# Optimization experiments

Hardware: AMD Instinct MI355X
Metric: run time of the kernel (lower is better)

## Reference

```python
import jax, jax.numpy as jnp
import numpy as np

H = 64  # hidden size


def _gru_cell(x, h, Wih, Whh, bih, bhh):
    """PyTorch-convention GRU cell. x:[B,in], h:[B,H]. Gate order: r, z, n."""
    gi = x @ Wih.T + bih              # [B, 3H]
    gh = h @ Whh.T + bhh              # [B, 3H]
    ir, iz, in_ = jnp.split(gi, 3, axis=-1)
    hr, hz, hn = jnp.split(gh, 3, axis=-1)
    r = jax.nn.sigmoid(ir + hr)
    z = jax.nn.sigmoid(iz + hz)
    n = jnp.tanh(in_ + r * hn)
    return (1.0 - z) * n + z * h


def setup_inputs() -> dict:
    key = jax.random.key(0)
    B, T, NIN = 4096, 256, 6
    ks = jax.random.split(key, 24)

    def w(k, shape, fan):
        return (jax.random.normal(k, shape, jnp.float32) / np.sqrt(fan).astype(np.float32))

    inp = {"x": jax.random.normal(ks[0], (B, T, NIN), jnp.float32)}
    # encoder layer 0 (input 6) and layer 1 (input 64)
    inp["enc_Wih0"] = w(ks[1], (3 * H, NIN), H)
    inp["enc_Whh0"] = w(ks[2], (3 * H, H), H)
    inp["enc_bih0"] = w(ks[3], (3 * H,), H)
    inp["enc_bhh0"] = w(ks[4], (3 * H,), H)
    inp["enc_Wih1"] = w(ks[5], (3 * H, H), H)
    inp["enc_Whh1"] = w(ks[6], (3 * H, H), H)
    inp["enc_bih1"] = w(ks[7], (3 * H,), H)
    inp["enc_bhh1"] = w(ks[8], (3 * H,), H)
    # decoder layer 0 (input 1) and layer 1 (input 64)
    inp["dec_Wih0"] = w(ks[9], (3 * H, 1), H)
    inp["dec_Whh0"] = w(ks[10], (3 * H, H), H)
    inp["dec_bih0"] = w(ks[11], (3 * H,), H)
    inp["dec_bhh0"] = w(ks[12], (3 * H,), H)
    inp["dec_Wih1"] = w(ks[13], (3 * H, H), H)
    inp["dec_Whh1"] = w(ks[14], (3 * H, H), H)
    inp["dec_bih1"] = w(ks[15], (3 * H,), H)
    inp["dec_bhh1"] = w(ks[16], (3 * H,), H)
    # output head
    inp["out_W"] = w(ks[17], (1, H), H)
    inp["out_b"] = w(ks[18], (1,), H)
    inp["target_len"] = 180
    return inp


def reference(x, enc_Wih0, enc_Whh0, enc_bih0, enc_bhh0,
              enc_Wih1, enc_Whh1, enc_bih1, enc_bhh1,
              dec_Wih0, dec_Whh0, dec_bih0, dec_bhh0,
              dec_Wih1, dec_Whh1, dec_bih1, dec_bhh1,
              out_W, out_b, target_len):
    B = x.shape[0]
    dtype = x.dtype

    # ---- encoder: 2-layer GRU over x, return final hidden per layer ----
    seq = jnp.swapaxes(x, 0, 1)  # [T, B, 6] time-major
    enc_layers = [(enc_Wih0, enc_Whh0, enc_bih0, enc_bhh0),
                  (enc_Wih1, enc_Whh1, enc_bih1, enc_bhh1)]
    h_finals = []
    for (Wih, Whh, bih, bhh) in enc_layers:
        def step(h, xt, Wih=Wih, Whh=Whh, bih=bih, bhh=bhh):
            hn = _gru_cell(xt, h, Wih, Whh, bih, bhh)
            return hn, hn
        h_last, seq = jax.lax.scan(step, jnp.zeros((B, H), dtype), seq)
        h_finals.append(h_last)

    def dec_step(carry, _):
        h0, h1, prev = carry
        h0 = _gru_cell(prev, h0, dec_Wih0, dec_Whh0, dec_bih0, dec_bhh0)
        h1 = _gru_cell(h0, h1, dec_Wih1, dec_Whh1, dec_bih1, dec_bhh1)
        cv = h1 @ out_W.T + out_b  # [B, 1]
        return (h0, h1, cv), cv

    prev0 = jnp.zeros((B, 1), dtype)
    _, outs = jax.lax.scan(dec_step, (h_finals[0], h_finals[1], prev0),
                           None, length=target_len)
    return jnp.swapaxes(outs, 0, 1)  # [B, target_len, 1]
```

## Files before the change

### kernel.cpp

```cpp
#include <hip/hip_runtime.h>
#include <cstdint>

typedef _Float16 half8 __attribute__((ext_vector_type(8)));
typedef __attribute__((ext_vector_type(4))) float floatx4;
typedef unsigned int uint;

#define TSEQ 256
#define TDEC 180
#define NIN  6
#define GROWS 16
#define NBLK (4096 / GROWS)
#define NSL 4
#define RS0 104
#define RS1 72
#define L2E 1.4426950408889634f

__device__ __forceinline__ floatx4 mfma16(half8 a, half8 b, floatx4 c) {
  return __builtin_amdgcn_mfma_f32_16x16x32_f16(a, b, c, 0, 0, 0);
}

__device__ __forceinline__ float sigm2(float v) {
  return __builtin_amdgcn_rcpf(1.0f + __builtin_amdgcn_exp2f(-v));
}
__device__ __forceinline__ float tanh2(float v) {
  return fmaf(2.0f, __builtin_amdgcn_rcpf(1.0f + __builtin_amdgcn_exp2f(-v)), -1.0f);
}

__device__ __forceinline__ half8 ldh8(const _Float16* p) { return *(const half8*)p; }

#define PASS2_I3(F0, F1, r, z, g, W, QR, QZ, QG) do {                   \
  r = mfma16(F0, W[0][0], QR); z = mfma16(F0, W[1][0], QZ); g = mfma16(F0, W[2][0], QG); \
  r = mfma16(F1, W[0][1], r);  z = mfma16(F1, W[1][1], z);  g = mfma16(F1, W[2][1], g);  \
} while (0)

#define PASS2_A2I1(F0, F1, r, z, g, W, QG) do {                         \
  r = mfma16(F0, W[0][0], r); z = mfma16(F0, W[1][0], z); g = mfma16(F0, W[2][0], QG); \
  r = mfma16(F1, W[0][1], r); z = mfma16(F1, W[1][1], z); g = mfma16(F1, W[2][1], g);  \
} while (0)

#define PASS1_A2I1(F0, r, z, g, W, QG) do {                             \
  r = mfma16(F0, W[0][0], r); z = mfma16(F0, W[1][0], z); g = mfma16(F0, W[2][0], QG); \
} while (0)

__device__ __forceinline__ void pollge1(const volatile uint* p, uint need4) {
  for (;;) {
    if (*p >= need4) break;
    __builtin_amdgcn_s_sleep(1);
  }
  asm volatile("" ::: "memory");
}

#define PUBLISH() do { asm volatile("" ::: "memory"); if (lane == 0) atomicAdd(mysum, 1u); } while (0)

__global__ void __launch_bounds__(512, 2)
gru_persist(const float* __restrict__ x,
            const float* __restrict__ eWih0, const float* __restrict__ eWhh0,
            const float* __restrict__ ebih0, const float* __restrict__ ebhh0,
            const float* __restrict__ eWih1, const float* __restrict__ eWhh1,
            const float* __restrict__ ebih1, const float* __restrict__ ebhh1,
            const float* __restrict__ dWih0, const float* __restrict__ dWhh0,
            const float* __restrict__ dbih0, const float* __restrict__ dbhh0,
            const float* __restrict__ dWih1, const float* __restrict__ dWhh1,
            const float* __restrict__ dbih1, const float* __restrict__ dbhh1,
            const float* __restrict__ outW, const float* __restrict__ outB,
            float* __restrict__ out)
{
  __shared__ __align__(16) _Float16 s0[NSL][16][RS0];
  __shared__ __align__(16) _Float16 s1[NSL][16][RS1];
  __shared__ __align__(16) uint prog[16];

  const int tid  = threadIdx.x;
  const bool isA = tid < 256;
  const int wvL  = (tid >> 6) & 3;
  const int lane = tid & 63;
  const int c    = lane & 15;
  const int q    = lane >> 4;
  const int u    = wvL * 16 + c;
  const long base = (long)blockIdx.x * GROWS;

  const volatile uint* asum = (const volatile uint*)&prog[0];
  const volatile uint* bsum = (const volatile uint*)&prog[8];
  uint* mysum = (uint*)&prog[isA ? 0 : 8];

  for (int i = tid; i < NSL * 16 * RS0; i += 512) ((uint16_t*)s0)[i] = 0;
  for (int i = tid; i < NSL * 16 * RS1; i += 512) ((uint16_t*)s1)[i] = 0;
  if (tid < 16) prog[tid] = 0;
  if (tid < GROWS * NIN) {
    int m = tid / 6, i2 = tid - m * 6;
    s0[0][m][64 + i2] = (_Float16)x[(base + m) * (TSEQ * NIN) + i2];
  }

  half8 W1[3][2], W2[3][2];
  half8 W1d[3][2], W2d[3][2];
  float hr[4] = {0, 0, 0, 0};
  const float SC[3] = {L2E, L2E, 2.0f * L2E};

  auto loadW64 = [&](const float* W, half8 (&D)[3][2]) {
    #pragma unroll
    for (int s = 0; s < 3; s++) {
      const int n = (s * 4 + wvL) * 16 + c;
      #pragma unroll
      for (int kt = 0; kt < 2; kt++) {
        const int k0 = kt * 32 + q * 8;
        #pragma unroll
        for (int j = 0; j < 8; j++) D[s][kt][j] = (_Float16)(SC[s] * W[n * 64 + k0 + j]);
      }
    }
  };

  const float ob = outB[0];
  float cR, cZ, c3, c4;
  float dR, dZ, d3, d4;
  float bR0 = 0, bZ0 = 0, b30 = 0, b40 = 0;
  float wk[2][8];
  if (isA) {
    loadW64(eWhh0, W1);
    #pragma unroll
    for (int s = 0; s < 3; s++) {
      const int n = (s * 4 + wvL) * 16 + c;
      #pragma unroll
      for (int kt = 0; kt < 2; kt++)
        #pragma unroll
        for (int j = 0; j < 8; j++) {
          float v = (kt == 0 && q == 0 && j < NIN) ? SC[s] * eWih0[n * NIN + j] : 0.0f;
          W2[s][kt][j] = (_Float16)v;
        }
    }
    loadW64(dWhh0, W1d);
    #pragma unroll
    for (int s = 0; s < 3; s++) {
      const int n = (s * 4 + wvL) * 16 + c;
      const float wd = SC[s] * dWih0[n];
      #pragma unroll
      for (int kt = 0; kt < 2; kt++) {
        const int k0 = kt * 32 + q * 8;
        #pragma unroll
        for (int j = 0; j < 8; j++) W2d[s][kt][j] = (_Float16)(wd * outW[k0 + j]);
      }
    }
    cR = L2E * (ebih0[u] + ebhh0[u]);
    cZ = L2E * (ebih0[64 + u] + ebhh0[64 + u]);
    c3 = 2.0f * L2E * ebhh0[128 + u];
    c4 = 2.0f * L2E * ebih0[128 + u];
    bR0 = L2E * (dbih0[u] + dbhh0[u]);
    bZ0 = L2E * (dbih0[64 + u] + dbhh0[64 + u]);
    b30 = 2.0f * L2E * dbhh0[128 + u];
    b40 = 2.0f * L2E * dbih0[128 + u];
    dR = bR0 + L2E * (dWih0[u] * ob);
    dZ = bZ0 + L2E * (dWih0[64 + u] * ob);
    d3 = b30;
    d4 = b40 + 2.0f * L2E * (dWih0[128 + u] * ob);
  } else {
    loadW64(eWih1, W1); loadW64(eWhh1, W2);
    loadW64(dWih1, W1d); loadW64(dWhh1, W2d);
    cR = L2E * (ebih1[u] + ebhh1[u]);
    cZ = L2E * (ebih1[64 + u] + ebhh1[64 + u]);
    c3 = 2.0f * L2E * ebih1[128 + u];
    c4 = 2.0f * L2E * ebhh1[128 + u];
    dR = L2E * (dbih1[u] + dbhh1[u]);
    dZ = L2E * (dbih1[64 + u] + dbhh1[64 + u]);
    d3 = 2.0f * L2E * dbih1[128 + u];
    d4 = 2.0f * L2E * dbhh1[128 + u];
    #pragma unroll
    for (int kt = 0; kt < 2; kt++)
      #pragma unroll
      for (int j = 0; j < 8; j++) wk[kt][j] = outW[kt * 32 + q * 8 + j];
  }
  __syncthreads();

  if (isA) {
    floatx4 QR = {cR, cR, cR, cR}, QZ = {cZ, cZ, cZ, cZ};
    floatx4 Q3 = {c3, c3, c3, c3}, Q4 = {c4, c4, c4, c4};
    const bool doX = (wvL == 0) && (lane < 48);
    const float *px0 = nullptr, *px1 = nullptr;
    int xo0 = 0, xo1 = 0;
    float xa0 = 0.f, xa1 = 0.f, xb0 = 0.f, xb1 = 0.f;
    if (doX) {
      int s0_ = lane, s1_ = lane + 48;
      int m0 = s0_ / 6, i0 = s0_ - m0 * 6, m1 = s1_ / 6, i1 = s1_ - m1 * 6;
      px0 = x + (base + m0) * (TSEQ * NIN) + i0;
      px1 = x + (base + m1) * (TSEQ * NIN) + i1;
      xo0 = m0 * RS0 + 64 + i0; xo1 = m1 * RS0 + 64 + i1;
      xa0 = px0[NIN];     xa1 = px1[NIN];
      xb0 = px0[2 * NIN]; xb1 = px1[2 * NIN];
    }
    for (int i = 0; i < TSEQ; i += 4) {
      #pragma unroll
      for (int h4 = 0; h4 < 4; h4++) {
        const int i_ = i + h4, p = h4, pn = (h4 + 1) & 3;
        pollge1(asum, 4u * (uint)i_);
        const half8 a0 = ldh8(&s0[p][c][q * 8]);
        const half8 a1 = ldh8(&s0[p][c][32 + q * 8]);
        const half8 xf = ldh8(&s0[p][c][64 + q * 8]);
        floatx4 aR, aZ, a3, a4;
        PASS2_I3(a0, a1, aR, aZ, a3, W1, QR, QZ, Q3);
        PASS1_A2I1(xf, aR, aZ, a4, W2, Q4);
        pollge1(bsum, 4u * (uint)(i_ > 3 ? i_ - 3 : 0));
        if (doX && i_ + 1 < TSEQ) {
          ((_Float16*)s0[pn])[xo0] = (_Float16)xa0;
          ((_Float16*)s0[pn])[xo1] = (_Float16)xa1;
          xa0 = xb0; xa1 = xb1;
          if (i_ + 3 < TSEQ) { xb0 = px0[(i_ + 3) * NIN]; xb1 = px1[(i_ + 3) * NIN]; }
        }
        #pragma unroll
        for (int r4 = 0; r4 < 4; r4++) {
          const float gr = sigm2(aR[r4]);
          const float gz = sigm2(aZ[r4]);
          const float nn = tanh2(a4[r4] + gr * a3[r4]);
          const float hn = nn + gz * (hr[r4] - nn);
          hr[r4] = hn;
          s0[pn][q * 4 + r4][u] = (_Float16)hn;
        }
        PUBLISH();
      }
    }
    QR = (floatx4){dR, dR, dR, dR}; QZ = (floatx4){dZ, dZ, dZ, dZ};
    Q3 = (floatx4){d3, d3, d3, d3}; Q4 = (floatx4){d4, d4, d4, d4};
    {
      pollge1(asum, 4u * (uint)TSEQ);
      const half8 a0 = ldh8(&s0[0][c][q * 8]);
      const half8 a1 = ldh8(&s0[0][c][32 + q * 8]);
      const floatx4 TR = {bR0, bR0, bR0, bR0}, TZ = {bZ0, bZ0, bZ0, bZ0};
      const floatx4 T3 = {b30, b30, b30, b30};
      floatx4 aR, aZ, a3;
      floatx4 a4 = {b40, b40, b40, b40};
      PASS2_I3(a0, a1, aR, aZ, a3, W1d, TR, TZ, T3);
      pollge1(bsum, 4u * (uint)(TSEQ - 1));
      #pragma unroll
      for (int r4 = 0; r4 < 4; r4++) {
        const float gr = sigm2(aR[r4]);
        const float gz = sigm2(aZ[r4]);
        const float nn = tanh2(a4[r4] + gr * a3[r4]);
        const float hn = nn + gz * (hr[r4] - nn);
        hr[r4] = hn;
        s0[1][q * 4 + r4][u] = (_Float16)hn;
      }
      PUBLISH();
    }
    for (int i_ = TSEQ + 1; i_ < TSEQ + TDEC; i_++) {
      const int p = i_ & 3, pn = (i_ + 1) & 3;
      pollge1(asum, 4u * (uint)i_);
      const half8 a0 = ldh8(&s0[p][c][q * 8]);
      const half8 a1 = ldh8(&s0[p][c][32 + q * 8]);
      floatx4 aR, aZ, a3, a4;
      PASS2_I3(a0, a1, aR, aZ, a3, W1d, QR, QZ, Q3);
      pollge1(bsum, 4u * (uint)i_);
      const half8 b0 = ldh8(&s1[p][c][q * 8]);
      const half8 b1 = ldh8(&s1[p][c][32 + q * 8]);
      PASS2_A2I1(b0, b1, aR, aZ, a4, W2d, Q4);
      #pragma unroll
      for (int r4 = 0; r4 < 4; r4++) {
        const float gr = sigm2(aR[r4]);
        const float gz = sigm2(aZ[r4]);
        const float nn = tanh2(a4[r4] + gr * a3[r4]);
        const float hn = nn + gz * (hr[r4] - nn);
        hr[r4] = hn;
        s0[pn][q * 4 + r4][u] = (_Float16)hn;
      }
      PUBLISH();
    }
  } else {
    floatx4 QR = {cR, cR, cR, cR}, QZ = {cZ, cZ, cZ, cZ};
    floatx4 Q3 = {c3, c3, c3, c3}, Q4 = {c4, c4, c4, c4};
    for (int i = 0; i < TSEQ; i += 4) {
      #pragma unroll
      for (int h4 = 0; h4 < 4; h4++) {
        const int i_ = i + h4, p = h4, pn = (h4 + 1) & 3;
        pollge1(bsum, 4u * (uint)i_);
        const half8 f0 = ldh8(&s1[p][c][q * 8]);
        const half8 f1 = ldh8(&s1[p][c][32 + q * 8]);
        floatx4 aR, aZ, a3, a4;
        PASS2_I3(f0, f1, aR, aZ, a4, W2, QR, QZ, Q4);
        pollge1(asum, 4u * (uint)(i_ + 1));
        const half8 g0 = ldh8(&s0[pn][c][q * 8]);
        const half8 g1 = ldh8(&s0[pn][c][32 + q * 8]);
        PASS2_A2I1(g0, g1, aR, aZ, a3, W1, Q3);
        #pragma unroll
        for (int r4 = 0; r4 < 4; r4++) {
          const float gr = sigm2(aR[r4]);
          const float gz = sigm2(aZ[r4]);
          const float nn = tanh2(a3[r4] + gr * a4[r4]);
          const float hn = nn + gz * (hr[r4] - nn);
          hr[r4] = hn;
          s1[pn][q * 4 + r4][u] = (_Float16)hn;
        }
        PUBLISH();
      }
    }
    QR = (floatx4){dR, dR, dR, dR}; QZ = (floatx4){dZ, dZ, dZ, dZ};
    Q3 = (floatx4){d3, d3, d3, d3}; Q4 = (floatx4){d4, d4, d4, d4};
    for (int i_ = TSEQ; i_ < TSEQ + TDEC; i_++) {
      const int p = i_ & 3, pn = (i_ + 1) & 3;
      pollge1(bsum, 4u * (uint)i_);
      const half8 f0 = ldh8(&s1[p][c][q * 8]);
      const half8 f1 = ldh8(&s1[p][c][32 + q * 8]);
      floatx4 aR, aZ, a3, a4;
      PASS2_I3(f0, f1, aR, aZ, a4, W2d, QR, QZ, Q4);
      if (wvL == 0 && i_ > TSEQ) {
        float cv = 0.0f;
        #pragma unroll
        for (int j = 0; j < 8; j++) {
          cv = fmaf((float)f0[j], wk[0][j], cv);
          cv = fmaf((float)f1[j], wk[1][j], cv);
        }
        cv += __shfl_xor(cv, 16);
        cv += __shfl_xor(cv, 32);
        if (lane < 16) out[(base + lane) * TDEC + (i_ - TSEQ - 1)] = cv + ob;
      }
      pollge1(asum, 4u * (uint)(i_ + 1));
      const half8 g0 = ldh8(&s0[pn][c][q * 8]);
      const half8 g1 = ldh8(&s0[pn][c][32 + q * 8]);
      PASS2_A2I1(g0, g1, aR, aZ, a3, W1d, Q3);
      #pragma unroll
      for (int r4 = 0; r4 < 4; r4++) {
        const float gr = sigm2(aR[r4]);
        const float gz = sigm2(aZ[r4]);
        const float nn = tanh2(a3[r4] + gr * a4[r4]);
        const float hn = nn + gz * (hr[r4] - nn);
        hr[r4] = hn;
        s1[pn][q * 4 + r4][u] = (_Float16)hn;
      }
      PUBLISH();
    }
    if (wvL == 0) {
      pollge1(bsum, 4u * (uint)(TSEQ + TDEC));
      const half8 f0 = ldh8(&s1[0][c][q * 8]);
      const half8 f1 = ldh8(&s1[0][c][32 + q * 8]);
      float cv = 0.0f;
      #pragma unroll
      for (int j = 0; j < 8; j++) {
        cv = fmaf((float)f0[j], wk[0][j], cv);
        cv = fmaf((float)f1[j], wk[1][j], cv);
      }
      cv += __shfl_xor(cv, 16);
      cv += __shfl_xor(cv, 32);
      if (lane < 16) out[(base + lane) * TDEC + (TDEC - 1)] = cv + ob;
    }
  }
}

extern "C" void kernel_launch(void* const* d_in, const int* in_sizes, int n_in,
                              void* d_out, int out_size, void* d_ws, size_t ws_size,
                              hipStream_t stream) {
  (void)in_sizes; (void)n_in; (void)d_ws; (void)ws_size; (void)out_size;
  const float* x     = (const float*)d_in[0];
  const float* eWih0 = (const float*)d_in[1];
  const float* eWhh0 = (const float*)d_in[2];
  const float* ebih0 = (const float*)d_in[3];
  const float* ebhh0 = (const float*)d_in[4];
  const float* eWih1 = (const float*)d_in[5];
  const float* eWhh1 = (const float*)d_in[6];
  const float* ebih1 = (const float*)d_in[7];
  const float* ebhh1 = (const float*)d_in[8];
  const float* dWih0 = (const float*)d_in[9];
  const float* dWhh0 = (const float*)d_in[10];
  const float* dbih0 = (const float*)d_in[11];
  const float* dbhh0 = (const float*)d_in[12];
  const float* dWih1 = (const float*)d_in[13];
  const float* dWhh1 = (const float*)d_in[14];
  const float* dbih1 = (const float*)d_in[15];
  const float* dbhh1 = (const float*)d_in[16];
  const float* outW  = (const float*)d_in[17];
  const float* outB  = (const float*)d_in[18];
  hipLaunchKernelGGL(gru_persist, dim3(NBLK), dim3(512), 0, stream,
                     x, eWih0, eWhh0, ebih0, ebhh0, eWih1, eWhh1, ebih1, ebhh1,
                     dWih0, dWhh0, dbih0, dbhh0, dWih1, dWhh1, dbih1, dbhh1,
                     outW, outB, (float*)d_out);
}
```

Measured before the change: 387.2 us.

## Replace LDS counter polling with workgroup barriers in a lockstep wavefront schedule

Drops the shared-memory progress counters, the sleep-polling loops and the atomic publishes between the layer-0 and layer-1 wave groups. All 8 waves now advance in lockstep with s_barrier, and the layer-1 schedule is skewed by one step through peeled prologue and epilogue iterations, so that matching barrier counts line up between the two groups. This removes atomic and polling latency, but loses the slack that let layer 0 run up to several steps ahead of layer 1. Mismatched barrier counts between the two branches would deadlock or race.

```diff
diff --git a/kernel.cpp b/kernel.cpp
--- a/kernel.cpp
+++ b/kernel.cpp
@@ -3,7 +3,6 @@
 
 typedef _Float16 half8 __attribute__((ext_vector_type(8)));
 typedef __attribute__((ext_vector_type(4))) float floatx4;
-typedef unsigned int uint;
 
 #define TSEQ 256
 #define TDEC 180
@@ -42,15 +41,11 @@
   r = mfma16(F0, W[0][0], r); z = mfma16(F0, W[1][0], z); g = mfma16(F0, W[2][0], QG); \
 } while (0)
 
-__device__ __forceinline__ void pollge1(const volatile uint* p, uint need4) {
-  for (;;) {
-    if (*p >= need4) break;
-    __builtin_amdgcn_s_sleep(1);
-  }
-  asm volatile("" ::: "memory");
-}
-
-#define PUBLISH() do { asm volatile("" ::: "memory"); if (lane == 0) atomicAdd(mysum, 1u); } while (0)
+#define SYNC() do {                                         \
+  asm volatile("s_waitcnt lgkmcnt(0)" ::: "memory");        \
+  __builtin_amdgcn_s_barrier();                             \
+  asm volatile("" ::: "memory");                            \
+} while (0)
 
 __global__ void __launch_bounds__(512, 2)
 gru_persist(const float* __restrict__ x,
@@ -67,7 +62,6 @@
 {
   __shared__ __align__(16) _Float16 s0[NSL][16][RS0];
   __shared__ __align__(16) _Float16 s1[NSL][16][RS1];
-  __shared__ __align__(16) uint prog[16];
 
   const int tid  = threadIdx.x;
   const bool isA = tid < 256;
@@ -78,13 +72,8 @@
   const int u    = wvL * 16 + c;
   const long base = (long)blockIdx.x * GROWS;
 
-  const volatile uint* asum = (const volatile uint*)&prog[0];
-  const volatile uint* bsum = (const volatile uint*)&prog[8];
-  uint* mysum = (uint*)&prog[isA ? 0 : 8];
-
   for (int i = tid; i < NSL * 16 * RS0; i += 512) ((uint16_t*)s0)[i] = 0;
   for (int i = tid; i < NSL * 16 * RS1; i += 512) ((uint16_t*)s1)[i] = 0;
-  if (tid < 16) prog[tid] = 0;
   if (tid < GROWS * NIN) {
     int m = tid / 6, i2 = tid - m * 6;
     s0[0][m][64 + i2] = (_Float16)x[(base + m) * (TSEQ * NIN) + i2];
@@ -184,18 +173,16 @@
       xa0 = px0[NIN];     xa1 = px1[NIN];
       xb0 = px0[2 * NIN]; xb1 = px1[2 * NIN];
     }
-    for (int i = 0; i < TSEQ; i += 4) {
+    for (int k = 0; k < TSEQ; k += 4) {
       #pragma unroll
       for (int h4 = 0; h4 < 4; h4++) {
-        const int i_ = i + h4, p = h4, pn = (h4 + 1) & 3;
-        pollge1(asum, 4u * (uint)i_);
+        const int i_ = k + h4, p = h4, pn = (h4 + 1) & 3;
         const half8 a0 = ldh8(&s0[p][c][q * 8]);
         const half8 a1 = ldh8(&s0[p][c][32 + q * 8]);
         const half8 xf = ldh8(&s0[p][c][64 + q * 8]);
         floatx4 aR, aZ, a3, a4;
         PASS2_I3(a0, a1, aR, aZ, a3, W1, QR, QZ, Q3);
         PASS1_A2I1(xf, aR, aZ, a4, W2, Q4);
-        pollge1(bsum, 4u * (uint)(i_ > 3 ? i_ - 3 : 0));
         if (doX && i_ + 1 < TSEQ) {
           ((_Float16*)s0[pn])[xo0] = (_Float16)xa0;
           ((_Float16*)s0[pn])[xo1] = (_Float16)xa1;
@@ -211,13 +198,10 @@
           hr[r4] = hn;
           s0[pn][q * 4 + r4][u] = (_Float16)hn;
         }
-        PUBLISH();
-      }
-    }
-    QR = (floatx4){dR, dR, dR, dR}; QZ = (floatx4){dZ, dZ, dZ, dZ};
-    Q3 = (floatx4){d3, d3, d3, d3}; Q4 = (floatx4){d4, d4, d4, d4};
+        SYNC();
+      }
+    }
     {
-      pollge1(asum, 4u * (uint)TSEQ);
       const half8 a0 = ldh8(&s0[0][c][q * 8]);
       const half8 a1 = ldh8(&s0[0][c][32 + q * 8]);
       const floatx4 TR = {bR0, bR0, bR0, bR0}, TZ = {bZ0, bZ0, bZ0, bZ0};
@@ -225,7 +209,6 @@
       floatx4 aR, aZ, a3;
       floatx4 a4 = {b40, b40, b40, b40};
       PASS2_I3(a0, a1, aR, aZ, a3, W1d, TR, TZ, T3);
-      pollge1(bsum, 4u * (uint)(TSEQ - 1));
       #pragma unroll
       for (int r4 = 0; r4 < 4; r4++) {
         const float gr = sigm2(aR[r4]);
@@ -235,16 +218,17 @@
         hr[r4] = hn;
         s0[1][q * 4 + r4][u] = (_Float16)hn;
       }
-      PUBLISH();
-    }
+      SYNC();
+    }
+    QR = (floatx4){dR, dR, dR, dR}; QZ = (floatx4){dZ, dZ, dZ, dZ};
+    Q3 = (floatx4){d3, d3, d3, d3}; Q4 = (floatx4){d4, d4, d4, d4};
     for (int i_ = TSEQ + 1; i_ < TSEQ + TDEC; i_++) {
       const int p = i_ & 3, pn = (i_ + 1) & 3;
-      pollge1(asum, 4u * (uint)i_);
       const half8 a0 = ldh8(&s0[p][c][q * 8]);
       const half8 a1 = ldh8(&s0[p][c][32 + q * 8]);
       floatx4 aR, aZ, a3, a4;
       PASS2_I3(a0, a1, aR, aZ, a3, W1d, QR, QZ, Q3);
-      pollge1(bsum, 4u * (uint)i_);
+      SYNC();
       const half8 b0 = ldh8(&s1[p][c][q * 8]);
       const half8 b1 = ldh8(&s1[p][c][32 + q * 8]);
       PASS2_A2I1(b0, b1, aR, aZ, a4, W2d, Q4);
@@ -257,46 +241,85 @@
         hr[r4] = hn;
         s0[pn][q * 4 + r4][u] = (_Float16)hn;
       }
-      PUBLISH();
-    }
+      SYNC();
+    }
+    SYNC();
   } else {
     floatx4 QR = {cR, cR, cR, cR}, QZ = {cZ, cZ, cZ, cZ};
     floatx4 Q3 = {c3, c3, c3, c3}, Q4 = {c4, c4, c4, c4};
-    for (int i = 0; i < TSEQ; i += 4) {
+    for (int k = 0; k < TSEQ; k += 4) {
       #pragma unroll
       for (int h4 = 0; h4 < 4; h4++) {
-        const int i_ = i + h4, p = h4, pn = (h4 + 1) & 3;
-        pollge1(bsum, 4u * (uint)i_);
-        const half8 f0 = ldh8(&s1[p][c][q * 8]);
-        const half8 f1 = ldh8(&s1[p][c][32 + q * 8]);
-        floatx4 aR, aZ, a3, a4;
-        PASS2_I3(f0, f1, aR, aZ, a4, W2, QR, QZ, Q4);
-        pollge1(asum, 4u * (uint)(i_ + 1));
-        const half8 g0 = ldh8(&s0[pn][c][q * 8]);
-        const half8 g1 = ldh8(&s0[pn][c][32 + q * 8]);
-        PASS2_A2I1(g0, g1, aR, aZ, a3, W1, Q3);
-        #pragma unroll
-        for (int r4 = 0; r4 < 4; r4++) {
-          const float gr = sigm2(aR[r4]);
-          const float gz = sigm2(aZ[r4]);
-          const float nn = tanh2(a3[r4] + gr * a4[r4]);
-          const float hn = nn + gz * (hr[r4] - nn);
-          hr[r4] = hn;
-          s1[pn][q * 4 + r4][u] = (_Float16)hn;
-        }
-        PUBLISH();
-      }
+        const int kk = k + h4;
+        if (kk > 0) {
+          const int p = (h4 + 3) & 3, pn = h4;
+          const half8 f0 = ldh8(&s1[p][c][q * 8]);
+          const half8 f1 = ldh8(&s1[p][c][32 + q * 8]);
+          floatx4 aR, aZ, a3, a4;
+          PASS2_I3(f0, f1, aR, aZ, a4, W2, QR, QZ, Q4);
+          const half8 g0 = ldh8(&s0[pn][c][q * 8]);
+          const half8 g1 = ldh8(&s0[pn][c][32 + q * 8]);
+          PASS2_A2I1(g0, g1, aR, aZ, a3, W1, Q3);
+          #pragma unroll
+          for (int r4 = 0; r4 < 4; r4++) {
+            const float gr = sigm2(aR[r4]);
+            const float gz = sigm2(aZ[r4]);
+            const float nn = tanh2(a3[r4] + gr * a4[r4]);
+            const float hn = nn + gz * (hr[r4] - nn);
+            hr[r4] = hn;
+            s1[pn][q * 4 + r4][u] = (_Float16)hn;
+          }
+        }
+        SYNC();
+      }
+    }
+    {
+      const half8 f0 = ldh8(&s1[3][c][q * 8]);
+      const half8 f1 = ldh8(&s1[3][c][32 + q * 8]);
+      floatx4 aR, aZ, a3, a4;
+      PASS2_I3(f0, f1, aR, aZ, a4, W2, QR, QZ, Q4);
+      const half8 g0 = ldh8(&s0[0][c][q * 8]);
+      const half8 g1 = ldh8(&s0[0][c][32 + q * 8]);
+      PASS2_A2I1(g0, g1, aR, aZ, a3, W1, Q3);
+      #pragma unroll
+      for (int r4 = 0; r4 < 4; r4++) {
+        const float gr = sigm2(aR[r4]);
+        const float gz = sigm2(aZ[r4]);
+        const float nn = tanh2(a3[r4] + gr * a4[r4]);
+        const float hn = nn + gz * (hr[r4] - nn);
+        hr[r4] = hn;
+        s1[0][q * 4 + r4][u] = (_Float16)hn;
+      }
+      SYNC();
     }
     QR = (floatx4){dR, dR, dR, dR}; QZ = (floatx4){dZ, dZ, dZ, dZ};
     Q3 = (floatx4){d3, d3, d3, d3}; Q4 = (floatx4){d4, d4, d4, d4};
-    for (int i_ = TSEQ; i_ < TSEQ + TDEC; i_++) {
+    {
+      const half8 f0 = ldh8(&s1[0][c][q * 8]);
+      const half8 f1 = ldh8(&s1[0][c][32 + q * 8]);
+      floatx4 aR, aZ, a3, a4;
+      PASS2_I3(f0, f1, aR, aZ, a4, W2d, QR, QZ, Q4);
+      const half8 g0 = ldh8(&s0[1][c][q * 8]);
+      const half8 g1 = ldh8(&s0[1][c][32 + q * 8]);
+      PASS2_A2I1(g0, g1, aR, aZ, a3, W1d, Q3);
+      #pragma unroll
+      for (int r4 = 0; r4 < 4; r4++) {
+        const float gr = sigm2(aR[r4]);
+        const float gz = sigm2(aZ[r4]);
+        const float nn = tanh2(a3[r4] + gr * a4[r4]);
+        const float hn = nn + gz * (hr[r4] - nn);
+        hr[r4] = hn;
+        s1[1][q * 4 + r4][u] = (_Float16)hn;
+      }
+      SYNC();
+    }
+    for (int i_ = TSEQ + 1; i_ < TSEQ + TDEC; i_++) {
       const int p = i_ & 3, pn = (i_ + 1) & 3;
-      pollge1(bsum, 4u * (uint)i_);
       const half8 f0 = ldh8(&s1[p][c][q * 8]);
       const half8 f1 = ldh8(&s1[p][c][32 + q * 8]);
       floatx4 aR, aZ, a3, a4;
       PASS2_I3(f0, f1, aR, aZ, a4, W2d, QR, QZ, Q4);
-      if (wvL == 0 && i_ > TSEQ) {
+      if (wvL == 0) {
         float cv = 0.0f;
         #pragma unroll
         for (int j = 0; j < 8; j++) {
@@ -307,7 +330,7 @@
         cv += __shfl_xor(cv, 32);
         if (lane < 16) out[(base + lane) * TDEC + (i_ - TSEQ - 1)] = cv + ob;
       }
-      pollge1(asum, 4u * (uint)(i_ + 1));
+      SYNC();
       const half8 g0 = ldh8(&s0[pn][c][q * 8]);
       const half8 g1 = ldh8(&s0[pn][c][32 + q * 8]);
       PASS2_A2I1(g0, g1, aR, aZ, a3, W1d, Q3);
@@ -320,10 +343,9 @@
         hr[r4] = hn;
         s1[pn][q * 4 + r4][u] = (_Float16)hn;
       }
-      PUBLISH();
+      SYNC();
     }
     if (wvL == 0) {
-      pollge1(bsum, 4u * (uint)(TSEQ + TDEC));
       const half8 f0 = ldh8(&s1[0][c][q * 8]);
       const half8 f1 = ldh8(&s1[0][c][32 + q * 8]);
       float cv = 0.0f;
```

Measured after the change: 360.6 us. 6.9% less time.
